# Kernel tuning notes

Measured on AMD Instinct MI355X. Metric: run time of the kernel, lower is better.

The kernel has to match this reference:

```python
import jax, jax.numpy as jnp
import numpy as np

B, C, H, W = 4, 96, 56, 56
K0, K1, DIL, HID = 5, 7, 3, 4  # HID: ConvMlp(dim, expansion, drop) => hidden_features = int(mlp_ratio) = 4 (repo quirk)
EPS = 1e-5


def _conv(x, w, b, pad, dil=1, groups=1):
    y = jax.lax.conv_general_dilated(x, w, (1, 1), [(pad, pad), (pad, pad)],
                                     rhs_dilation=(dil, dil),
                                     dimension_numbers=('NCHW', 'OIHW', 'NCHW'),
                                     feature_group_count=groups)
    return y + b[None, :, None, None]


def _conv1x1(x, w, b):
    return jnp.einsum('bchw,oc->bohw', x, w) + b[None, :, None, None]


def _ln(x, g, b):
    # LayerNormProxy: LayerNorm over channel dim of NCHW
    mu = jnp.mean(x, axis=1, keepdims=True)
    v = jnp.var(x, axis=1, keepdims=True)
    return (x - mu) * jax.lax.rsqrt(v + EPS) * g[None, :, None, None] + b[None, :, None, None]


def _gelu(x):
    return jax.nn.gelu(x, approximate=False)  # torch nn.GELU default = exact erf


def _deform_dw(x, ow, ob, dw, db, k, dil, pad):
    # DeformConv2d wrapper: offsets from a same-geometry conv, then depthwise deformable conv.
    Bx, Cx, Hx, Wx = x.shape
    P = k * k
    off = _conv(x, ow, ob, pad, dil).reshape(Bx, P, 2, Hx, Wx)  # [B,P,(y,x),H,W]
    ky = (jnp.repeat(jnp.arange(k), k) * dil - pad).astype(x.dtype)  # row-major kernel grid
    kx = (jnp.tile(jnp.arange(k), k) * dil - pad).astype(x.dtype)
    py = jnp.arange(Hx, dtype=x.dtype)[None, None, :, None] + ky[None, :, None, None] + off[:, :, 0]
    px = jnp.arange(Wx, dtype=x.dtype)[None, None, None, :] + kx[None, :, None, None] + off[:, :, 1]
    y0 = jnp.floor(py)
    x0 = jnp.floor(px)
    wy = py - y0
    wx = px - x0
    xf = x.reshape(Bx, Cx, Hx * Wx)

    def corner(yi, xi):
        valid = (yi >= 0) & (yi < Hx) & (xi >= 0) & (xi < Wx)
        idx = (jnp.clip(yi, 0, Hx - 1).astype(jnp.int32) * Wx
               + jnp.clip(xi, 0, Wx - 1).astype(jnp.int32)).reshape(Bx, -1)
        g = jax.vmap(lambda a, i: jnp.take(a, i, axis=1))(xf, idx).reshape(Bx, Cx, P, Hx, Wx)
        return g * valid[:, None].astype(x.dtype)

    v = (corner(y0, x0) * ((1 - wy) * (1 - wx))[:, None]
         + corner(y0, x0 + 1) * ((1 - wy) * wx)[:, None]
         + corner(y0 + 1, x0) * (wy * (1 - wx))[:, None]
         + corner(y0 + 1, x0 + 1) * (wy * wx)[:, None])  # [B,C,P,H,W]
    return jnp.einsum('bcphw,cp->bchw', v, dw) + db[None, :, None, None]


def setup_inputs() -> dict:
    key = jax.random.key(0)
    ks = iter(jax.random.split(key, 32))

    def rn(shape, s=1.0):
        return jax.random.normal(next(ks), shape, jnp.float32) * s

    f32 = jnp.float32
    return {
        'x': rn((B, C, H, W)),
        'g1n': jnp.ones((C,), f32), 'b1n': jnp.zeros((C,), f32),
        'p1w': rn((C, C), 1 / np.sqrt(C)), 'p1b': jnp.zeros((C,), f32),
        'o0w': rn((2 * K0 * K0, C, K0, K0), 0.05 / np.sqrt(C * K0 * K0)), 'o0b': jnp.zeros((2 * K0 * K0,), f32),
        'd0w': rn((C, K0 * K0), 1 / np.sqrt(K0 * K0)), 'd0b': jnp.zeros((C,), f32),
        'o1w': rn((2 * K1 * K1, C, K1, K1), 0.05 / np.sqrt(C * K1 * K1)), 'o1b': jnp.zeros((2 * K1 * K1,), f32),
        'd1w': rn((C, K1 * K1), 1 / np.sqrt(K1 * K1)), 'd1b': jnp.zeros((C,), f32),
        'c1w': rn((C, C), 1 / np.sqrt(C)), 'c1b': jnp.zeros((C,), f32),
        'p2w': rn((C, C), 1 / np.sqrt(C)), 'p2b': jnp.zeros((C,), f32),
        'ls1': jnp.full((C,), 0.01, f32),
        'g2n': jnp.ones((C,), f32), 'b2n': jnp.zeros((C,), f32),
        'f1w': rn((HID, C), 1 / np.sqrt(C)), 'f1b': jnp.zeros((HID,), f32),
        'dww': rn((HID, 1, 3, 3), 1 / 3.0), 'dwb': jnp.zeros((HID,), f32),
        'f2w': rn((C, HID), 1 / np.sqrt(HID)), 'f2b': jnp.zeros((C,), f32),
        'ls2': jnp.full((C,), 0.01, f32),
    }


def reference(x, g1n, b1n, p1w, p1b, o0w, o0b, d0w, d0b, o1w, o1b, d1w, d1b,
              c1w, c1b, p2w, p2b, ls1, g2n, b2n, f1w, f1b, dww, dwb, f2w, f2b, ls2):
    # attention branch
    y = _ln(x, g1n, b1n)
    shortcut = y
    y = _gelu(_conv1x1(y, p1w, p1b))
    u = y
    a = _deform_dw(y, o0w, o0b, d0w, d0b, K0, 1, K0 // 2)
    a = _deform_dw(a, o1w, o1b, d1w, d1b, K1, DIL, (K1 // 2) * DIL)
    a = _conv1x1(a, c1w, c1b)
    y = _conv1x1(u * a, p2w, p2b) + shortcut
    y = ls1[None, :, None, None] * y
    x = x + y
    # MLP branch (note: norm2 is applied to the branch output y, as in the source)
    z = _ln(y, g2n, b2n)
    z = _conv1x1(z, f1w, f1b)
    z = _gelu(_conv(z, dww, dwb, 1, 1, HID))
    z = _conv1x1(z, f2w, f2b)
    x = x + ls2[None, :, None, None] * z
    return x
```

## Files before the change

### kernel.cpp

```cpp
#include <hip/hip_runtime.h>
#include <math.h>

namespace {

constexpr int Bc = 4, Cc = 96, Hc = 56, Wc = 56;
constexpr int HWc = Hc * Wc;
constexpr int Nc  = Bc * HWc;
constexpr float EPSc = 1e-5f;

typedef __attribute__((ext_vector_type(8))) short bf16x8;
typedef __attribute__((ext_vector_type(4))) float f32x4;

__device__ __forceinline__ unsigned short f2bf(float f) {
  union { float f; unsigned u; } x; x.f = f;
  unsigned r = x.u + 0x7fffu + ((x.u >> 16) & 1u);
  return (unsigned short)(r >> 16);
}
__device__ __forceinline__ float bf2f(unsigned short u) {
  union { unsigned u; float f; } x; x.u = (unsigned)u << 16; return x.f;
}
__device__ __forceinline__ float gelu_exact(float x) {
  return 0.5f * x * (1.0f + erff(x * 0.7071067811865475f));
}

__global__ __launch_bounds__(256) void k_ln(const float* __restrict__ x,
                                            const float* __restrict__ g,
                                            const float* __restrict__ b,
                                            unsigned short* __restrict__ outN) {
  int pos = blockIdx.x * 256 + threadIdx.x;
  int bb = pos / HWc, hw = pos % HWc;
  const float* xb = x + (size_t)bb * Cc * HWc + hw;
  float s = 0.f, s2 = 0.f;
  for (int c = 0; c < Cc; ++c) { float v = xb[c * HWc]; s += v; s2 += v * v; }
  float mu  = s * (1.f / Cc);
  float var = fmaxf(s2 * (1.f / Cc) - mu * mu, 0.f);
  float rs  = rsqrtf(var + EPSc);
  unsigned short* ob = outN + (size_t)pos * Cc;
  for (int q = 0; q < 12; ++q) {
    unsigned short t8[8];
#pragma unroll
    for (int j = 0; j < 8; ++j) {
      int c = q * 8 + j;
      t8[j] = f2bf((xb[c * HWc] - mu) * rs * g[c] + b[c]);
    }
    *reinterpret_cast<bf16x8*>(ob + q * 8) = *reinterpret_cast<const bf16x8*>(t8);
  }
}

template <int K_, int MTILES, int P>
__global__ __launch_bounds__(256) void k_pack_w(const float* __restrict__ wsrc,
                                                unsigned short* __restrict__ wpk) {
  constexpr int TOTAL = K_ * K_ * 3 * MTILES * 512;
  int idx = blockIdx.x * 256 + threadIdx.x;
  if (idx >= TOTAL) return;
  int j    = idx & 7;
  int lane = (idx >> 3) & 63;
  int t    = idx >> 9;
  int mt   = t % MTILES;
  int step = t / MTILES;
  int o = mt * 16 + (lane & 15);
  int k = step * 32 + ((lane >> 4) & 3) * 8 + j;
  int p = k / Cc, c = k % Cc;
  float v = 0.f;
  if (o < P) v = wsrc[(((size_t)o * Cc + c) * K_ + p / K_) * K_ + (p % K_)];
  wpk[idx] = f2bf(v);
}

__global__ __launch_bounds__(256) void k_pack_dwt(const float* __restrict__ dwsrc,
                                                  float* __restrict__ dwt, int KK) {
  int idx = blockIdx.x * 256 + threadIdx.x;
  if (idx >= KK * Cc) return;
  int p = idx / Cc, c = idx % Cc;
  dwt[idx] = dwsrc[c * KK + p];
}

template <int GELU, int PADP, int WP>
__global__ __launch_bounds__(256) void k_pwg(const unsigned short* __restrict__ inN,
                                             const unsigned short* __restrict__ wpk,
                                             const float* __restrict__ bq,
                                             unsigned short* __restrict__ outPad) {
  int lane = threadIdx.x & 63;
  int wv = threadIdx.x >> 6;
  int ng = wv & 1, mg = wv >> 1;
  int n = blockIdx.x * 32 + ng * 16 + (lane & 15);
  int ko = ((lane >> 4) & 3) * 8;
  const unsigned short* ib = inN + (size_t)n * Cc + ko;
  const unsigned short* wl = wpk + (size_t)lane * 8;
  f32x4 acc[3];
#pragma unroll
  for (int m = 0; m < 3; ++m) acc[m] = (f32x4){0.f, 0.f, 0.f, 0.f};
#pragma unroll
  for (int ks = 0; ks < 3; ++ks) {
    bf16x8 bf = *reinterpret_cast<const bf16x8*>(ib + ks * 32);
#pragma unroll
    for (int m = 0; m < 3; ++m) {
      bf16x8 af = *reinterpret_cast<const bf16x8*>(wl + (size_t)(ks * 6 + mg * 3 + m) * 512);
      acc[m] = __builtin_amdgcn_mfma_f32_16x16x32_bf16(af, bf, acc[m], 0, 0, 0);
    }
  }
  int bb = n / HWc, hw = n % HWc;
  int h = hw / Wc, w = hw % Wc;
  unsigned short* ob = outPad + (((size_t)bb * (Hc + 2 * PADP) + h + PADP) * WP + w + PADP) * Cc;
  int orow = ((lane >> 4) & 3) * 4;
#pragma unroll
  for (int m = 0; m < 3; ++m) {
    int o0 = (mg * 3 + m) * 16 + orow;
    float4 bv = *reinterpret_cast<const float4*>(bq + o0);
    unsigned short t4[4];
#pragma unroll
    for (int j = 0; j < 4; ++j) {
      float r = acc[m][j] + ((const float*)&bv)[j];
      if (GELU) r = gelu_exact(r);
      t4[j] = f2bf(r);
    }
    *reinterpret_cast<uint2*>(ob + o0) = *reinterpret_cast<const uint2*>(t4);
  }
}

template <int UPADP, int UWP>
__global__ __launch_bounds__(256) void k_comb(const unsigned short* __restrict__ uPad,
                                              const unsigned short* __restrict__ An,
                                              const unsigned short* __restrict__ wpk,
                                              const float* __restrict__ bq,
                                              const unsigned short* __restrict__ ylnN,
                                              const float* __restrict__ ls1q,
                                              const float* __restrict__ x,
                                              float* __restrict__ out,
                                              unsigned short* __restrict__ y2N) {
  int lane = threadIdx.x & 63;
  int wv = threadIdx.x >> 6;
  int ng = wv & 1, mg = wv >> 1;
  int n = blockIdx.x * 32 + ng * 16 + (lane & 15);
  int ko = ((lane >> 4) & 3) * 8;
  int bb = n / HWc, hw = n % HWc;
  int h = hw / Wc, w = hw % Wc;
  const unsigned short* ub = uPad + (((size_t)bb * (Hc + 2 * UPADP) + h + UPADP) * UWP + w + UPADP) * Cc + ko;
  const unsigned short* ab = An + (size_t)n * Cc + ko;
  const unsigned short* wl = wpk + (size_t)lane * 8;
  f32x4 acc[3];
#pragma unroll
  for (int m = 0; m < 3; ++m) acc[m] = (f32x4){0.f, 0.f, 0.f, 0.f};
#pragma unroll
  for (int ks = 0; ks < 3; ++ks) {
    bf16x8 uv = *reinterpret_cast<const bf16x8*>(ub + ks * 32);
    bf16x8 av = *reinterpret_cast<const bf16x8*>(ab + ks * 32);
    union { bf16x8 v; unsigned short s[8]; } uu, aa, gg;
    uu.v = uv; aa.v = av;
#pragma unroll
    for (int j = 0; j < 8; ++j) gg.s[j] = f2bf(bf2f(uu.s[j]) * bf2f(aa.s[j]));
#pragma unroll
    for (int m = 0; m < 3; ++m) {
      bf16x8 af = *reinterpret_cast<const bf16x8*>(wl + (size_t)(ks * 6 + mg * 3 + m) * 512);
      acc[m] = __builtin_amdgcn_mfma_f32_16x16x32_bf16(af, gg.v, acc[m], 0, 0, 0);
    }
  }
  int orow = ((lane >> 4) & 3) * 4;
  const float* xb = x + (size_t)bb * Cc * HWc + hw;
  float* ob = out + (size_t)bb * Cc * HWc + hw;
#pragma unroll
  for (int m = 0; m < 3; ++m) {
    int o0 = (mg * 3 + m) * 16 + orow;
    float4 bv = *reinterpret_cast<const float4*>(bq + o0);
    float4 lv = *reinterpret_cast<const float4*>(ls1q + o0);
    uint2 yl = *reinterpret_cast<const uint2*>(ylnN + (size_t)n * Cc + o0);
    unsigned short yl4[4];
    *reinterpret_cast<uint2*>(yl4) = yl;
    unsigned short t4[4];
#pragma unroll
    for (int j = 0; j < 4; ++j) {
      float t = acc[m][j] + ((const float*)&bv)[j] + bf2f(yl4[j]);
      float y2 = ((const float*)&lv)[j] * t;
      t4[j] = f2bf(y2);
      ob[(size_t)(o0 + j) * HWc] = xb[(size_t)(o0 + j) * HWc] + y2;
    }
    *reinterpret_cast<uint2*>(y2N + (size_t)n * Cc + o0) = *reinterpret_cast<const uint2*>(t4);
  }
}

template <int K_, int DIL_, int MTILES, int MT, int P, int PADP, int WP, int PSTR>
__global__ __launch_bounds__(512) void k_conv_mfma(const unsigned short* __restrict__ inp,
                                                   const unsigned short* __restrict__ wpk,
                                                   const float* __restrict__ bq,
                                                   float* __restrict__ dstT) {
  constexpr int KK = K_ * K_;
  constexpr int HP = Hc + 2 * PADP;
  constexpr int NBLK = Nc / 32;
  int lane = threadIdx.x & 63;
  int wv = threadIdx.x >> 6;
  int nh = wv & 1, mg = wv >> 1;
  int bid = blockIdx.x;
  int ntile = (bid & 7) * (NBLK / 8) + (bid >> 3);
  int n = ntile * 32 + nh * 16 + (lane & 15);
  int b = n / HWc, hw = n % HWc;
  int h = hw / Wc, w = hw % Wc;
  int co = ((lane >> 4) & 3) * 8;
  const unsigned short* ib = inp + ((size_t)b * HP * WP + (size_t)h * WP + w) * Cc + co;
  const unsigned short* wl = wpk + (size_t)lane * 8;
  int mtc[MT];
#pragma unroll
  for (int i = 0; i < MT; ++i) mtc[i] = min(mg * MT + i, MTILES - 1);

  f32x4 acc[MT];
#pragma unroll
  for (int i = 0; i < MT; ++i) acc[i] = (f32x4){0.f, 0.f, 0.f, 0.f};

  bf16x8 B0[3], A0[MT][3], B1[3], A1[MT][3];

#define LOAD_TAP(Bb, Ab, pp)                                                          \
  {                                                                                   \
    size_t toff_ = (size_t)(((pp) / K_) * DIL_ * WP + ((pp) % K_) * DIL_) * Cc;       \
    _Pragma("unroll")                                                                 \
    for (int cc = 0; cc < 3; ++cc) {                                                  \
      Bb[cc] = *reinterpret_cast<const bf16x8*>(ib + toff_ + cc * 32);                \
      _Pragma("unroll")                                                               \
      for (int i = 0; i < MT; ++i)                                                    \
        Ab[i][cc] = *reinterpret_cast<const bf16x8*>(                                 \
            wl + ((size_t)((pp) * 3 + cc) * MTILES + mtc[i]) * 512);                  \
    }                                                                                 \
  }
#define MFMA_TAP(Bb, Ab)                                                              \
  {                                                                                   \
    _Pragma("unroll")                                                                 \
    for (int cc = 0; cc < 3; ++cc)                                                    \
      _Pragma("unroll")                                                               \
      for (int i = 0; i < MT; ++i)                                                    \
        acc[i] = __builtin_amdgcn_mfma_f32_16x16x32_bf16(Ab[i][cc], Bb[cc], acc[i],   \
                                                         0, 0, 0);                    \
  }

  LOAD_TAP(B0, A0, 0)
  LOAD_TAP(B1, A1, 1)
  for (int p = 0; p + 2 < KK; p += 2) {
    MFMA_TAP(B0, A0)
    LOAD_TAP(B0, A0, p + 2)
    MFMA_TAP(B1, A1)
    if (p + 3 < KK) LOAD_TAP(B1, A1, p + 3)
  }
  MFMA_TAP(B0, A0)
#undef LOAD_TAP
#undef MFMA_TAP

  int orow = ((lane >> 4) & 3) * 4;
#pragma unroll
  for (int i = 0; i < MT; ++i) {
    int mt = mg * MT + i;
    if (mt >= MTILES) break;
    float4 st;
#pragma unroll
    for (int j = 0; j < 4; ++j) {
      int o = mt * 16 + orow + j;
      float bias = (o < P) ? bq[o] : 0.f;
      ((float*)&st)[j] = acc[i][j] + bias;
    }
    *reinterpret_cast<float4*>(dstT + (size_t)n * PSTR + mt * 16 + orow) = st;
  }
}

template <int K_, int DIL_, int PAD_, int IPADP, int IWP, int OPADP, int OWP, int PSTR>
__global__ __launch_bounds__(256) void k_deform(const unsigned short* __restrict__ srcT,
                                                const float* __restrict__ offT,
                                                const float* __restrict__ dwt,
                                                const float* __restrict__ dbq,
                                                float* __restrict__ dst,
                                                unsigned short* __restrict__ dstPad) {
  constexpr int KK = K_ * K_;
  constexpr int KK4 = KK & ~3;
  constexpr int IHP = Hc + 2 * IPADP;
  int tid = blockIdx.x * 256 + threadIdx.x;
  int cg = tid % 24;
  int pos = tid / 24;
  int c = cg * 4;
  int bb = pos / HWc, hw = pos % HWc;
  int h = hw / Wc, w = hw % Wc;
  const unsigned short* sb = srcT + (size_t)bb * IHP * IWP * Cc + c;
  const float* ob = offT + (size_t)pos * PSTR;
  float ax = 0.f, ay = 0.f, az = 0.f, aw = 0.f;

  for (int pg = 0; pg < KK4; pg += 4) {
    float4 o01 = *reinterpret_cast<const float4*>(ob + 2 * pg);
    float4 o23 = *reinterpret_cast<const float4*>(ob + 2 * pg + 4);
    float oyv[4] = {o01.x, o01.z, o23.x, o23.z};
    float oxv[4] = {o01.y, o01.w, o23.y, o23.w};
    uint2 v[4][4];
    float wt[4][4];
#pragma unroll
    for (int i = 0; i < 4; ++i) {
      int p = pg + i;
      float py = (float)(h + (p / K_) * DIL_ - PAD_) + oyv[i];
      float px = (float)(w + (p % K_) * DIL_ - PAD_) + oxv[i];
      float y0f = floorf(py), x0f = floorf(px);
      float wy = py - y0f, wx = px - x0f;
      int y0 = (int)y0f, x0 = (int)x0f;
#pragma unroll
      for (int dy = 0; dy < 2; ++dy) {
        int yi = y0 + dy;
        bool yv = (unsigned)yi < (unsigned)Hc;
        int yc = min(max(yi, 0), Hc - 1);
        float wyv = dy ? wy : 1.f - wy;
#pragma unroll
        for (int dx = 0; dx < 2; ++dx) {
          int xi = x0 + dx;
          bool xv = (unsigned)xi < (unsigned)Wc;
          int xc = min(max(xi, 0), Wc - 1);
          wt[i][dy * 2 + dx] = (yv && xv) ? wyv * (dx ? wx : 1.f - wx) : 0.f;
          v[i][dy * 2 + dx] = *reinterpret_cast<const uint2*>(
              sb + ((size_t)(yc + IPADP) * IWP + (xc + IPADP)) * Cc);
        }
      }
    }
#pragma unroll
    for (int i = 0; i < 4; ++i) {
      int p = pg + i;
      float4 d = *reinterpret_cast<const float4*>(dwt + (size_t)p * Cc + c);
      float sx = 0.f, sy = 0.f, sz = 0.f, sw = 0.f;
#pragma unroll
      for (int q = 0; q < 4; ++q) {
        float wq_ = wt[i][q];
        sx += wq_ * bf2f((unsigned short)(v[i][q].x & 0xffffu));
        sy += wq_ * bf2f((unsigned short)(v[i][q].x >> 16));
        sz += wq_ * bf2f((unsigned short)(v[i][q].y & 0xffffu));
        sw += wq_ * bf2f((unsigned short)(v[i][q].y >> 16));
      }
      ax += sx * d.x; ay += sy * d.y; az += sz * d.z; aw += sw * d.w;
    }
  }
  {
    int p = KK - 1;
    float oy = ob[2 * p], ox = ob[2 * p + 1];
    float py = (float)(h + (p / K_) * DIL_ - PAD_) + oy;
    float px = (float)(w + (p % K_) * DIL_ - PAD_) + ox;
    float y0f = floorf(py), x0f = floorf(px);
    float wy = py - y0f, wx = px - x0f;
    int y0 = (int)y0f, x0 = (int)x0f;
    uint2 v[4]; float wt[4];
#pragma unroll
    for (int dy = 0; dy < 2; ++dy) {
      int yi = y0 + dy;
      bool yv = (unsigned)yi < (unsigned)Hc;
      int yc = min(max(yi, 0), Hc - 1);
      float wyv = dy ? wy : 1.f - wy;
#pragma unroll
      for (int dx = 0; dx < 2; ++dx) {
        int xi = x0 + dx;
        bool xv = (unsigned)xi < (unsigned)Wc;
        int xc = min(max(xi, 0), Wc - 1);
        wt[dy * 2 + dx] = (yv && xv) ? wyv * (dx ? wx : 1.f - wx) : 0.f;
        v[dy * 2 + dx] = *reinterpret_cast<const uint2*>(
            sb + ((size_t)(yc + IPADP) * IWP + (xc + IPADP)) * Cc);
      }
    }
    float4 d = *reinterpret_cast<const float4*>(dwt + (size_t)p * Cc + c);
    float sx = 0.f, sy = 0.f, sz = 0.f, sw = 0.f;
#pragma unroll
    for (int q = 0; q < 4; ++q) {
      sx += wt[q] * bf2f((unsigned short)(v[q].x & 0xffffu));
      sy += wt[q] * bf2f((unsigned short)(v[q].x >> 16));
      sz += wt[q] * bf2f((unsigned short)(v[q].y & 0xffffu));
      sw += wt[q] * bf2f((unsigned short)(v[q].y >> 16));
    }
    ax += sx * d.x; ay += sy * d.y; az += sz * d.z; aw += sw * d.w;
  }

  ax += dbq[c]; ay += dbq[c + 1]; az += dbq[c + 2]; aw += dbq[c + 3];
  if (dst) {
    float* d = dst + (size_t)bb * Cc * HWc + hw;
    d[(c + 0) * HWc] = ax; d[(c + 1) * HWc] = ay;
    d[(c + 2) * HWc] = az; d[(c + 3) * HWc] = aw;
  }
  if (dstPad) {
    unsigned short t4[4] = {f2bf(ax), f2bf(ay), f2bf(az), f2bf(aw)};
    unsigned short* tb = dstPad + (((size_t)bb * (Hc + 2 * OPADP) + h + OPADP) * OWP + w + OPADP) * Cc + c;
    *reinterpret_cast<uint2*>(tb) = *reinterpret_cast<const uint2*>(t4);
  }
}

__global__ __launch_bounds__(256) void k_mlp1(const unsigned short* __restrict__ y2N,
                                              const float* __restrict__ g,
                                              const float* __restrict__ b,
                                              const float* __restrict__ f1wq,
                                              const float* __restrict__ f1bq,
                                              float* __restrict__ z4) {
  int pos = blockIdx.x * 256 + threadIdx.x;
  int bb = pos / HWc, hw = pos % HWc;
  const unsigned short* yb = y2N + (size_t)pos * Cc;
  float vv[96];
  float s = 0.f, s2 = 0.f;
#pragma unroll
  for (int q = 0; q < 12; ++q) {
    bf16x8 t = *reinterpret_cast<const bf16x8*>(yb + q * 8);
    union { bf16x8 v; unsigned short s[8]; } u; u.v = t;
#pragma unroll
    for (int j = 0; j < 8; ++j) {
      float f = bf2f(u.s[j]);
      vv[q * 8 + j] = f; s += f; s2 += f * f;
    }
  }
  float mu  = s * (1.f / Cc);
  float var = fmaxf(s2 * (1.f / Cc) - mu * mu, 0.f);
  float rs  = rsqrtf(var + EPSc);
  float a0 = 0.f, a1 = 0.f, a2 = 0.f, a3 = 0.f;
#pragma unroll
  for (int c = 0; c < 96; ++c) {
    float t = (vv[c] - mu) * rs * g[c] + b[c];
    a0 += t * f1wq[0 * Cc + c];
    a1 += t * f1wq[1 * Cc + c];
    a2 += t * f1wq[2 * Cc + c];
    a3 += t * f1wq[3 * Cc + c];
  }
  float* zb = z4 + (size_t)bb * 4 * HWc + hw;
  zb[0 * HWc] = a0 + f1bq[0];
  zb[1 * HWc] = a1 + f1bq[1];
  zb[2 * HWc] = a2 + f1bq[2];
  zb[3 * HWc] = a3 + f1bq[3];
}

__global__ __launch_bounds__(256) void k_mlp_dw(const float* __restrict__ z4,
                                                const float* __restrict__ dwwq,
                                                const float* __restrict__ dwbq,
                                                float* __restrict__ z4b) {
  int tid = blockIdx.x * 256 + threadIdx.x;
  int hw = tid % HWc;
  int bj = tid / HWc;
  int j = bj % 4;
  int h = hw / Wc, w = hw % Wc;
  const float* zb = z4 + (size_t)bj * HWc;
  float s = 0.f;
#pragma unroll
  for (int ky = 0; ky < 3; ++ky) {
    int y = h + ky - 1;
    if ((unsigned)y >= (unsigned)Hc) continue;
#pragma unroll
    for (int kx = 0; kx < 3; ++kx) {
      int x = w + kx - 1;
      if ((unsigned)x >= (unsigned)Wc) continue;
      s += zb[y * Wc + x] * dwwq[j * 9 + ky * 3 + kx];
    }
  }
  z4b[tid] = gelu_exact(s + dwbq[j]);
}

__global__ __launch_bounds__(256) void k_mlp2(const float* __restrict__ z4b,
                                              const float* __restrict__ f2wq,
                                              const float* __restrict__ f2bq,
                                              const float* __restrict__ ls2q,
                                              float* __restrict__ out) {
  int pos = blockIdx.x * 256 + threadIdx.x;
  int bb = pos / HWc, hw = pos % HWc;
  const float* zb = z4b + (size_t)bb * 4 * HWc + hw;
  float z0 = zb[0 * HWc], z1 = zb[1 * HWc], z2 = zb[2 * HWc], z3 = zb[3 * HWc];
  float* ob = out + (size_t)bb * Cc * HWc + hw;
  for (int o = 0; o < Cc; ++o) {
    float s = f2bq[o] + z0 * f2wq[o * 4 + 0] + z1 * f2wq[o * 4 + 1]
                      + z2 * f2wq[o * 4 + 2] + z3 * f2wq[o * 4 + 3];
    ob[o * HWc] += ls2q[o] * s;
  }
}

}

extern "C" void kernel_launch(void* const* d_in, const int* in_sizes, int n_in,
                              void* d_out, int out_size, void* d_ws, size_t ws_size,
                              hipStream_t stream) {
  (void)in_sizes; (void)n_in; (void)out_size; (void)ws_size;
  const float* x   = (const float*)d_in[0];
  const float* g1n = (const float*)d_in[1];
  const float* b1n = (const float*)d_in[2];
  const float* p1w = (const float*)d_in[3];
  const float* p1b = (const float*)d_in[4];
  const float* o0w = (const float*)d_in[5];
  const float* o0b = (const float*)d_in[6];
  const float* d0w = (const float*)d_in[7];
  const float* d0b = (const float*)d_in[8];
  const float* o1w = (const float*)d_in[9];
  const float* o1b = (const float*)d_in[10];
  const float* d1w = (const float*)d_in[11];
  const float* d1b = (const float*)d_in[12];
  const float* c1w = (const float*)d_in[13];
  const float* c1b = (const float*)d_in[14];
  const float* p2w = (const float*)d_in[15];
  const float* p2b = (const float*)d_in[16];
  const float* ls1 = (const float*)d_in[17];
  const float* g2n = (const float*)d_in[18];
  const float* b2n = (const float*)d_in[19];
  const float* f1w = (const float*)d_in[20];
  const float* f1b = (const float*)d_in[21];
  const float* dww = (const float*)d_in[22];
  const float* dwb = (const float*)d_in[23];
  const float* f2w = (const float*)d_in[24];
  const float* f2b = (const float*)d_in[25];
  const float* ls2 = (const float*)d_in[26];
  float* out = (float*)d_out;
  float* ws  = (float*)d_ws;

  float* off0t = ws;                                  size_t o_ = (size_t)Nc * 64;
  float* off1t = ws + o_;                             o_ += (size_t)Nc * 112;
  float* z4    = ws + o_;                             o_ += (size_t)Bc * 4 * HWc;
  float* z4b   = ws + o_;                             o_ += (size_t)Bc * 4 * HWc;
  float* dwt0  = ws + o_;                             o_ += 25 * Cc;
  float* dwt1  = ws + o_;                             o_ += 49 * Cc;
  unsigned short* yln_n  = (unsigned short*)(ws + o_); o_ += (size_t)Nc * Cc / 2;
  unsigned short* a1_n   = (unsigned short*)(ws + o_); o_ += (size_t)Nc * Cc / 2;
  unsigned short* A_n    = (unsigned short*)(ws + o_); o_ += (size_t)Nc * Cc / 2;
  unsigned short* y2_n   = (unsigned short*)(ws + o_); o_ += (size_t)Nc * Cc / 2;
  unsigned short* u_pad  = (unsigned short*)(ws + o_); o_ += (size_t)Bc * 60 * 60 * Cc / 2;
  unsigned short* a0_pad = (unsigned short*)(ws + o_); o_ += (size_t)Bc * 74 * 74 * Cc / 2;
  unsigned short* wpk0   = (unsigned short*)(ws + o_); o_ += (size_t)25 * 3 * 4 * 512 / 2;
  unsigned short* wpk1   = (unsigned short*)(ws + o_); o_ += (size_t)49 * 3 * 7 * 512 / 2;
  unsigned short* wpkp1  = (unsigned short*)(ws + o_); o_ += (size_t)3 * 6 * 512 / 2;
  unsigned short* wpkc1  = (unsigned short*)(ws + o_); o_ += (size_t)3 * 6 * 512 / 2;
  unsigned short* wpkp2  = (unsigned short*)(ws + o_); o_ += (size_t)3 * 6 * 512 / 2;

  dim3 b256(256, 1, 1), b512(512, 1, 1);

  hipMemsetAsync(u_pad, 0, (size_t)Bc * 60 * 60 * Cc * sizeof(unsigned short), stream);
  hipMemsetAsync(a0_pad, 0, (size_t)Bc * 74 * 74 * Cc * sizeof(unsigned short), stream);
  hipLaunchKernelGGL((k_pack_w<5, 4, 50>), dim3((25 * 3 * 4 * 512 + 255) / 256), b256, 0, stream, o0w, wpk0);
  hipLaunchKernelGGL((k_pack_w<7, 7, 98>), dim3((49 * 3 * 7 * 512 + 255) / 256), b256, 0, stream, o1w, wpk1);
  hipLaunchKernelGGL((k_pack_w<1, 6, 96>), dim3((3 * 6 * 512 + 255) / 256), b256, 0, stream, p1w, wpkp1);
  hipLaunchKernelGGL((k_pack_w<1, 6, 96>), dim3((3 * 6 * 512 + 255) / 256), b256, 0, stream, c1w, wpkc1);
  hipLaunchKernelGGL((k_pack_w<1, 6, 96>), dim3((3 * 6 * 512 + 255) / 256), b256, 0, stream, p2w, wpkp2);
  hipLaunchKernelGGL(k_pack_dwt, dim3((25 * Cc + 255) / 256), b256, 0, stream, d0w, dwt0, 25);
  hipLaunchKernelGGL(k_pack_dwt, dim3((49 * Cc + 255) / 256), b256, 0, stream, d1w, dwt1, 49);

  hipLaunchKernelGGL(k_ln, dim3(Nc / 256), b256, 0, stream, x, g1n, b1n, yln_n);
  hipLaunchKernelGGL((k_pwg<1, 2, 60>), dim3(Nc / 32), b256, 0, stream, yln_n, wpkp1, p1b, u_pad);
  hipLaunchKernelGGL((k_conv_mfma<5, 1, 4, 1, 50, 2, 60, 64>), dim3(Nc / 32), b512, 0, stream,
                     u_pad, wpk0, o0b, off0t);
  hipLaunchKernelGGL((k_deform<5, 1, 2, 2, 60, 9, 74, 64>), dim3(Nc * 24 / 256), b256, 0, stream,
                     u_pad, off0t, dwt0, d0b, (float*)nullptr, a0_pad);
  hipLaunchKernelGGL((k_conv_mfma<7, 3, 7, 2, 98, 9, 74, 112>), dim3(Nc / 32), b512, 0, stream,
                     a0_pad, wpk1, o1b, off1t);
  hipLaunchKernelGGL((k_deform<7, 3, 9, 9, 74, 0, 56, 112>), dim3(Nc * 24 / 256), b256, 0, stream,
                     a0_pad, off1t, dwt1, d1b, (float*)nullptr, a1_n);
  hipLaunchKernelGGL((k_pwg<0, 0, 56>), dim3(Nc / 32), b256, 0, stream, a1_n, wpkc1, c1b, A_n);
  hipLaunchKernelGGL((k_comb<2, 60>), dim3(Nc / 32), b256, 0, stream,
                     u_pad, A_n, wpkp2, p2b, yln_n, ls1, x, out, y2_n);
  hipLaunchKernelGGL(k_mlp1, dim3(Nc / 256), b256, 0, stream, y2_n, g2n, b2n, f1w, f1b, z4);
  hipLaunchKernelGGL(k_mlp_dw, dim3(Nc * 4 / 256), b256, 0, stream, z4, dww, dwb, z4b);
  hipLaunchKernelGGL(k_mlp2, dim3(Nc / 256), b256, 0, stream, z4b, f2w, f2b, ls2, out);
}
```

Baseline: 243.1 us.

## Reuse weight fragments across two pixel tiles per wave in offset conv

Each wave of the offset-conv MFMA kernel now computes both 16-pixel halves of the 32-pixel tile, so every loaded weight fragment feeds two MFMAs. The block shrinks from 512 to 256 threads, which halves the waves sharing each output-tile group and cuts redundant weight loads. Scheduling barriers are placed between the load and MFMA phases to keep the double-buffered pipeline in order. The cost is more accumulator and operand registers per wave, which may lower occupancy.

```diff
diff --git a/kernel.cpp b/kernel.cpp
--- a/kernel.cpp
+++ b/kernel.cpp
@@ -178,7 +178,7 @@
 }
 
 template <int K_, int DIL_, int MTILES, int MT, int P, int PADP, int WP, int PSTR>
-__global__ __launch_bounds__(512) void k_conv_mfma(const unsigned short* __restrict__ inp,
+__global__ __launch_bounds__(256) void k_conv_mfma(const unsigned short* __restrict__ inp,
                                                    const unsigned short* __restrict__ wpk,
                                                    const float* __restrict__ bq,
                                                    float* __restrict__ dstT) {
@@ -187,31 +187,37 @@
   constexpr int NBLK = Nc / 32;
   int lane = threadIdx.x & 63;
   int wv = threadIdx.x >> 6;
-  int nh = wv & 1, mg = wv >> 1;
   int bid = blockIdx.x;
   int ntile = (bid & 7) * (NBLK / 8) + (bid >> 3);
-  int n = ntile * 32 + nh * 16 + (lane & 15);
-  int b = n / HWc, hw = n % HWc;
-  int h = hw / Wc, w = hw % Wc;
+  int n0 = ntile * 32 + (lane & 15);
+  int n1 = n0 + 16;
+  int b0 = n0 / HWc, hw0 = n0 % HWc, h0 = hw0 / Wc, w0 = hw0 % Wc;
+  int b1 = n1 / HWc, hw1 = n1 % HWc, h1 = hw1 / Wc, w1 = hw1 % Wc;
   int co = ((lane >> 4) & 3) * 8;
-  const unsigned short* ib = inp + ((size_t)b * HP * WP + (size_t)h * WP + w) * Cc + co;
+  const unsigned short* ib0 = inp + ((size_t)b0 * HP * WP + (size_t)h0 * WP + w0) * Cc + co;
+  const unsigned short* ib1 = inp + ((size_t)b1 * HP * WP + (size_t)h1 * WP + w1) * Cc + co;
   const unsigned short* wl = wpk + (size_t)lane * 8;
+  int mt0 = wv * MT;
   int mtc[MT];
 #pragma unroll
-  for (int i = 0; i < MT; ++i) mtc[i] = min(mg * MT + i, MTILES - 1);
-
-  f32x4 acc[MT];
-#pragma unroll
-  for (int i = 0; i < MT; ++i) acc[i] = (f32x4){0.f, 0.f, 0.f, 0.f};
-
-  bf16x8 B0[3], A0[MT][3], B1[3], A1[MT][3];
+  for (int i = 0; i < MT; ++i) mtc[i] = min(mt0 + i, MTILES - 1);
+
+  f32x4 acc[MT][2];
+#pragma unroll
+  for (int i = 0; i < MT; ++i) {
+    acc[i][0] = (f32x4){0.f, 0.f, 0.f, 0.f};
+    acc[i][1] = (f32x4){0.f, 0.f, 0.f, 0.f};
+  }
+
+  bf16x8 B0[3][2], A0[MT][3], B1[3][2], A1[MT][3];
 
 #define LOAD_TAP(Bb, Ab, pp)                                                          \
   {                                                                                   \
     size_t toff_ = (size_t)(((pp) / K_) * DIL_ * WP + ((pp) % K_) * DIL_) * Cc;       \
     _Pragma("unroll")                                                                 \
     for (int cc = 0; cc < 3; ++cc) {                                                  \
-      Bb[cc] = *reinterpret_cast<const bf16x8*>(ib + toff_ + cc * 32);                \
+      Bb[cc][0] = *reinterpret_cast<const bf16x8*>(ib0 + toff_ + cc * 32);            \
+      Bb[cc][1] = *reinterpret_cast<const bf16x8*>(ib1 + toff_ + cc * 32);            \
       _Pragma("unroll")                                                               \
       for (int i = 0; i < MT; ++i)                                                    \
         Ab[i][cc] = *reinterpret_cast<const bf16x8*>(                                 \
@@ -223,18 +229,24 @@
     _Pragma("unroll")                                                                 \
     for (int cc = 0; cc < 3; ++cc)                                                    \
       _Pragma("unroll")                                                               \
-      for (int i = 0; i < MT; ++i)                                                    \
-        acc[i] = __builtin_amdgcn_mfma_f32_16x16x32_bf16(Ab[i][cc], Bb[cc], acc[i],   \
-                                                         0, 0, 0);                    \
+      for (int i = 0; i < MT; ++i) {                                                  \
+        acc[i][0] = __builtin_amdgcn_mfma_f32_16x16x32_bf16(Ab[i][cc], Bb[cc][0],     \
+                                                            acc[i][0], 0, 0, 0);      \
+        acc[i][1] = __builtin_amdgcn_mfma_f32_16x16x32_bf16(Ab[i][cc], Bb[cc][1],     \
+                                                            acc[i][1], 0, 0, 0);      \
+      }                                                                               \
   }
 
   LOAD_TAP(B0, A0, 0)
   LOAD_TAP(B1, A1, 1)
-  for (int p = 0; p + 2 < KK; p += 2) {
+  int p = 0;
+  for (; p + 2 < KK; p += 2) {
     MFMA_TAP(B0, A0)
     LOAD_TAP(B0, A0, p + 2)
+    __builtin_amdgcn_sched_barrier(0);
     MFMA_TAP(B1, A1)
     if (p + 3 < KK) LOAD_TAP(B1, A1, p + 3)
+    __builtin_amdgcn_sched_barrier(0);
   }
   MFMA_TAP(B0, A0)
 #undef LOAD_TAP
@@ -243,16 +255,20 @@
   int orow = ((lane >> 4) & 3) * 4;
 #pragma unroll
   for (int i = 0; i < MT; ++i) {
-    int mt = mg * MT + i;
+    int mt = mt0 + i;
     if (mt >= MTILES) break;
-    float4 st;
-#pragma unroll
-    for (int j = 0; j < 4; ++j) {
-      int o = mt * 16 + orow + j;
-      float bias = (o < P) ? bq[o] : 0.f;
-      ((float*)&st)[j] = acc[i][j] + bias;
-    }
-    *reinterpret_cast<float4*>(dstT + (size_t)n * PSTR + mt * 16 + orow) = st;
+#pragma unroll
+    for (int nt = 0; nt < 2; ++nt) {
+      float4 st;
+#pragma unroll
+      for (int j = 0; j < 4; ++j) {
+        int o = mt * 16 + orow + j;
+        float bias = (o < P) ? bq[o] : 0.f;
+        ((float*)&st)[j] = acc[i][nt][j] + bias;
+      }
+      int n = nt ? n1 : n0;
+      *reinterpret_cast<float4*>(dstT + (size_t)n * PSTR + mt * 16 + orow) = st;
+    }
   }
 }
 
@@ -510,7 +526,7 @@
   unsigned short* wpkc1  = (unsigned short*)(ws + o_); o_ += (size_t)3 * 6 * 512 / 2;
   unsigned short* wpkp2  = (unsigned short*)(ws + o_); o_ += (size_t)3 * 6 * 512 / 2;
 
-  dim3 b256(256, 1, 1), b512(512, 1, 1);
+  dim3 b256(256, 1, 1);
 
   hipMemsetAsync(u_pad, 0, (size_t)Bc * 60 * 60 * Cc * sizeof(unsigned short), stream);
   hipMemsetAsync(a0_pad, 0, (size_t)Bc * 74 * 74 * Cc * sizeof(unsigned short), stream);
@@ -524,11 +540,11 @@
 
   hipLaunchKernelGGL(k_ln, dim3(Nc / 256), b256, 0, stream, x, g1n, b1n, yln_n);
   hipLaunchKernelGGL((k_pwg<1, 2, 60>), dim3(Nc / 32), b256, 0, stream, yln_n, wpkp1, p1b, u_pad);
-  hipLaunchKernelGGL((k_conv_mfma<5, 1, 4, 1, 50, 2, 60, 64>), dim3(Nc / 32), b512, 0, stream,
+  hipLaunchKernelGGL((k_conv_mfma<5, 1, 4, 1, 50, 2, 60, 64>), dim3(Nc / 32), b256, 0, stream,
                      u_pad, wpk0, o0b, off0t);
   hipLaunchKernelGGL((k_deform<5, 1, 2, 2, 60, 9, 74, 64>), dim3(Nc * 24 / 256), b256, 0, stream,
                      u_pad, off0t, dwt0, d0b, (float*)nullptr, a0_pad);
-  hipLaunchKernelGGL((k_conv_mfma<7, 3, 7, 2, 98, 9, 74, 112>), dim3(Nc / 32), b512, 0, stream,
+  hipLaunchKernelGGL((k_conv_mfma<7, 3, 7, 2, 98, 9, 74, 112>), dim3(Nc / 32), b256, 0, stream,
                      a0_pad, wpk1, o1b, off1t);
   hipLaunchKernelGGL((k_deform<7, 3, 9, 9, 74, 0, 56, 112>), dim3(Nc * 24 / 256), b256, 0, stream,
                      a0_pad, off1t, dwt1, d1b, (float*)nullptr, a1_n);
```

New measurement: 222.8 us. 8.3% less time.
